# Kernel optimization log

Measured on AMD Instinct MI355X. Metric: run time of the kernel, lower is better.

## Reference

```python
import jax, jax.numpy as jnp
import numpy as np

N_NODES = 50000
N_EDGES = 800000
VOCAB = 10000
EMB = 128
HID = 128
OUT = 128
N_GRAPHS = 512


def setup_inputs() -> dict:
    key = jax.random.key(0)
    ks = jax.random.split(key, 12)
    edge_index = jax.random.randint(ks[0], (2, N_EDGES), 0, N_NODES, dtype=jnp.int64 if jax.config.jax_enable_x64 else jnp.int32)
    features = jax.random.randint(ks[1], (N_NODES, 1), 0, VOCAB, dtype=jnp.int32)
    batch = jnp.sort(jax.random.randint(ks[2], (N_NODES,), 0, N_GRAPHS, dtype=jnp.int32))
    s = 0.02
    emb = jax.random.normal(ks[3], (VOCAB, EMB), dtype=jnp.float32) * s
    W1 = jax.random.normal(ks[4], (EMB, HID), dtype=jnp.float32) * (1.0 / np.sqrt(EMB))
    b1 = jnp.zeros((HID,), dtype=jnp.float32)
    W2 = jax.random.normal(ks[5], (HID, HID), dtype=jnp.float32) * (1.0 / np.sqrt(HID))
    b2 = jnp.zeros((HID,), dtype=jnp.float32)
    W3 = jax.random.normal(ks[6], (HID, OUT), dtype=jnp.float32) * (1.0 / np.sqrt(HID))
    b3 = jnp.zeros((OUT,), dtype=jnp.float32)
    fcW = jax.random.normal(ks[7], (OUT, 1), dtype=jnp.float32) * (1.0 / np.sqrt(OUT))
    fcb = jnp.zeros((1,), dtype=jnp.float32)
    return dict(edge_index=edge_index, features=features, batch=batch,
                emb=emb, W1=W1, b1=b1, W2=W2, b2=b2, W3=W3, b3=b3,
                fcW=fcW, fcb=fcb)


def _gcn_conv(x, W, b, src, dst):
    # PyG GCNConv: add self-loops, symmetric deg^{-1/2} normalization,
    # linear transform first (no bias), then normalized scatter-add, then + bias.
    x = x @ W                                                    # [N, F_out]
    deg = jax.ops.segment_sum(jnp.ones((src.shape[0],), x.dtype), dst,
                              num_segments=N_NODES) + 1.0        # +1 self-loop
    dinv = jax.lax.rsqrt(deg)                                    # [N]
    norm = dinv[src] * dinv[dst]                                 # [E]
    msg = x[src] * norm[:, None]                                 # [E, F_out] gather
    agg = jax.ops.segment_sum(msg, dst, num_segments=N_NODES)    # scatter-add
    agg = agg + x * (dinv * dinv)[:, None]                       # self-loop term
    return agg + b


def reference(edge_index, features, batch, emb, W1, b1, W2, b2, W3, b3, fcW, fcb):
    src, dst = edge_index[0], edge_index[1]
    x = emb[features[:, 0]]                                      # [N, EMB]
    x = jax.nn.relu(_gcn_conv(x, W1, b1, src, dst))
    x = jax.nn.relu(_gcn_conv(x, W2, b2, src, dst))
    x = jax.nn.relu(_gcn_conv(x, W3, b3, src, dst))
    # global mean pool over graphs
    sums = jax.ops.segment_sum(x, batch, num_segments=N_GRAPHS)  # [G, OUT]
    cnts = jax.ops.segment_sum(jnp.ones((N_NODES,), x.dtype), batch,
                               num_segments=N_GRAPHS)
    pooled = sums / jnp.maximum(cnts, 1.0)[:, None]
    return (pooled @ fcW + fcb)[:, 0]                            # [G]
```

## Files before the change

kernel.cpp:

```cpp
#include <hip/hip_runtime.h>
#include <hip/hip_fp16.h>

#define N_NODES 50000
#define N_EDGES 800000
#define N_GRAPHS 512
#define VOCAB 10000
#define C 128
#define NBUCK 196
#define A_BLOCKS 200
#define EDGES_PER_A (N_EDGES / A_BLOCKS)
#define SE_CAP 8192

typedef __attribute__((ext_vector_type(8))) short short8v;
typedef __attribute__((ext_vector_type(4))) float f32x4;

__device__ __forceinline__ unsigned short f2bf(float f){
  unsigned u = __builtin_bit_cast(unsigned, f);
  unsigned r = u + 0x7FFFu + ((u >> 16) & 1u);
  return (unsigned short)(r >> 16);
}
__device__ __forceinline__ float bf2f(unsigned short h){
  unsigned u = ((unsigned)h) << 16;
  return __builtin_bit_cast(float, u);
}
__device__ __forceinline__ float h2f(short s){
  return __half2float(__builtin_bit_cast(__half, (unsigned short)s));
}

__global__ __launch_bounds__(256) void k_pre(const int* __restrict__ dst, int* __restrict__ blockHist,
                      const int* __restrict__ batch, int* __restrict__ gStart,
                      const float* __restrict__ W1, const float* __restrict__ W2,
                      const float* __restrict__ W3, short* __restrict__ Bp,
                      const float* __restrict__ emb, __half* __restrict__ embh){
  __shared__ int h[256];
  int b = blockIdx.x, t = threadIdx.x;
  if (b < A_BLOCKS){
    h[t] = 0; __syncthreads();
    int base = b * EDGES_PER_A;
    for (int i = t; i < EDGES_PER_A; i += 256)
      atomicAdd(&h[dst[base+i] >> 8], 1);
    __syncthreads();
    blockHist[t*A_BLOCKS + b] = h[t];
  } else if (b < A_BLOCKS+NBUCK){
    int i = (b-A_BLOCKS)*256 + t;
    if (i >= N_NODES) return;
    int bb = batch[i];
    int pb = (i==0) ? -1 : batch[i-1];
    for (int g=pb+1; g<=bb; g++) gStart[g] = i;
    if (i == N_NODES-1)
      for (int g=bb+1; g<=N_GRAPHS; g++) gStart[g] = N_NODES;
  } else if (b < A_BLOCKS+NBUCK+24){
    int idx = (b-A_BLOCKS-NBUCK)*256 + t;
    int layer = idx / 2048;
    int r = idx - layer*2048;
    const float* W = (layer==0) ? W1 : (layer==1) ? W2 : W3;
    short* Bh = Bp + (size_t)layer*32768;
    short* Bl = Bh + 16384;
    int lane = r & 63, tile = r >> 6;
    int kt = tile >> 3, ct = tile & 7;
    int q = lane >> 4, c = ct*16 + (lane & 15);
    #pragma unroll
    for (int i=0;i<8;i++){
      int k = kt*32 + q*8 + i;
      float w = W[k*C + c];
      unsigned short hh = f2bf(w);
      unsigned short ll = f2bf(w - bf2f(hh));
      Bh[(size_t)(tile*64 + lane)*8 + i] = (short)hh;
      Bl[(size_t)(tile*64 + lane)*8 + i] = (short)ll;
    }
  } else {
    int idx = (b-A_BLOCKS-NBUCK-24)*256 + t;
    const float2* s = (const float2*)emb;
    __half2* d2 = (__half2*)embh;
    for (int i = idx; i < VOCAB*C/2; i += 64*256)
      d2[i] = __float22half2_rn(s[i]);
  }
}

__global__ __launch_bounds__(64) void k_binScanA(const int* __restrict__ blockHist,
                        int* __restrict__ blockOfs, int* __restrict__ bucketTot){
  int b = blockIdx.x;
  int l = threadIdx.x;
  int carry = 0;
  for (int c = 0; c < 256; c += 64){
    int idx = c + l;
    int v = (idx < A_BLOCKS) ? blockHist[b*A_BLOCKS + idx] : 0;
    int x = v;
    #pragma unroll
    for (int off=1; off<64; off<<=1){
      int y = __shfl_up(x, off);
      if (l >= off) x += y;
    }
    if (idx < A_BLOCKS) blockOfs[b*A_BLOCKS + idx] = carry + x - v;
    carry += __shfl(x, 63);
  }
  if (l == 0) bucketTot[b] = carry;
}

__global__ __launch_bounds__(256) void k_binScatter(const int* __restrict__ src, const int* __restrict__ dst,
                           const int* __restrict__ bucketTot, const int* __restrict__ blockOfs,
                           unsigned* __restrict__ binned){
  __shared__ int s[256], ofs[256], cur[256];
  int t = threadIdx.x;
  int tv = bucketTot[t];
  s[t] = tv; __syncthreads();
  for (int off=1; off<256; off<<=1){
    int u = (t>=off) ? s[t-off] : 0;
    __syncthreads();
    s[t] += u;
    __syncthreads();
  }
  ofs[t] = (s[t] - tv) + blockOfs[t*A_BLOCKS + blockIdx.x];
  cur[t] = 0;
  __syncthreads();
  int base = blockIdx.x * EDGES_PER_A;
  for (int i = t; i < EDGES_PER_A; i += 256){
    int d = dst[base+i];
    int b = d >> 8;
    int p = atomicAdd(&cur[b], 1);
    binned[ofs[b] + p] = (unsigned)(src[base+i] & 0xFFFF) | ((unsigned)(d & 0xFF) << 16);
  }
}

__global__ __launch_bounds__(256) void k_binFinal(const unsigned* __restrict__ binned,
                         const int* __restrict__ bucketTot, const int* __restrict__ feat,
                         unsigned short* __restrict__ eSrc, unsigned short* __restrict__ eFeat,
                         int* __restrict__ rowStart, int* __restrict__ deg, float* __restrict__ dinv){
  __shared__ int h[256], pre[256], cur[256], excl[256];
  __shared__ unsigned short sE[SE_CAP];
  int b = blockIdx.x;
  int t = threadIdx.x;
  int tv = bucketTot[t];
  pre[t] = tv; __syncthreads();
  for (int off=1; off<256; off<<=1){
    int u = (t>=off) ? pre[t-off] : 0;
    __syncthreads();
    pre[t] += u;
    __syncthreads();
  }
  excl[t] = pre[t] - tv;
  __syncthreads();
  int base = excl[b], cnt = bucketTot[b];
  int nodeBase = b << 8;
  h[t] = 0; __syncthreads();
  for (int i = t; i < cnt; i += 256)
    atomicAdd(&h[binned[base+i] >> 16], 1);
  __syncthreads();
  pre[t] = h[t]; __syncthreads();
  for (int off=1; off<256; off<<=1){
    int u = (t>=off) ? pre[t-off] : 0;
    __syncthreads();
    pre[t] += u;
    __syncthreads();
  }
  int node = nodeBase + t;
  if (node < N_NODES){
    int d = h[t];
    deg[node] = d;
    rowStart[node] = base + pre[t] - d;
    dinv[node] = rsqrtf((float)d + 1.0f);
  }
  cur[t] = pre[t] - h[t];
  __syncthreads();
  for (int i = t; i < cnt; i += 256){
    unsigned v = binned[base+i];
    int dl = v >> 16;
    int p = atomicAdd(&cur[dl], 1);
    unsigned short s = (unsigned short)(v & 0xFFFF);
    if (p < SE_CAP) sE[p] = s;
    else eSrc[base + p] = s;
  }
  __syncthreads();
  int lim = cnt < SE_CAP ? cnt : SE_CAP;
  for (int i = t; i < lim; i += 256){
    unsigned short sv = sE[i];
    eSrc[base+i]  = sv;
    eFeat[base+i] = (unsigned short)feat[sv];
  }
  for (int i = SE_CAP + t; i < cnt; i += 256){
    eFeat[base+i] = (unsigned short)feat[eSrc[base+i]];
  }
}

__device__ __forceinline__ void store_split8(unsigned short* uh, unsigned short* ul,
                                             size_t node, int l16, const float* a){
  short8v hv, lv;
  #pragma unroll
  for (int i=0;i<8;i++){
    unsigned short hh = f2bf(a[i]);
    hv[i] = (short)hh;
    lv[i] = (short)f2bf(a[i] - bf2f(hh));
  }
  *(short8v*)&uh[node*C + l16*8] = hv;
  *(short8v*)&ul[node*C + l16*8] = lv;
}


__global__ __launch_bounds__(256) void k_agg1(const __half* __restrict__ embh,
                      const unsigned short* __restrict__ eSrc, const unsigned short* __restrict__ eFeat,
                      const int* __restrict__ rowStart, const int* __restrict__ deg,
                      const float* __restrict__ dinv, const int* __restrict__ feat,
                      unsigned short* __restrict__ uh, unsigned short* __restrict__ ul){
  int t = threadIdx.x;
  int wave = t>>6, lane = t&63;
  int sub = lane>>4, l16 = lane&15;
  int node = blockIdx.x*16 + wave*4 + sub;
  if (node >= N_NODES) return;
  int rs = rowStart[node], len = deg[node];
  float dn = dinv[node];
  const short8v* E = (const short8v*)embh;
  float a[8];
  {
    short8v v = E[(size_t)feat[node]*16 + l16];
    #pragma unroll
    for (int i=0;i<8;i++) a[i] = dn * h2f(v[i]);
  }
  int k = 0;
  for (; k+8<=len; k+=8){
    int f[8]; float dd[8];
    #pragma unroll
    for (int j=0;j<8;j++){
      int e = rs+k+j;
      f[j] = eFeat[e];
      dd[j] = dinv[eSrc[e]];
    }
    short8v v[8];
    #pragma unroll
    for (int j=0;j<8;j++) v[j] = E[(size_t)f[j]*16 + l16];
    #pragma unroll
    for (int j=0;j<8;j++)
      #pragma unroll
      for (int i=0;i<8;i++) a[i] = fmaf(dd[j], h2f(v[j][i]), a[i]);
  }
  for (; k<len; k++){
    float dd = dinv[eSrc[rs+k]];
    short8v v = E[(size_t)eFeat[rs+k]*16 + l16];
    #pragma unroll
    for (int i=0;i<8;i++) a[i] = fmaf(dd, h2f(v[i]), a[i]);
  }
  #pragma unroll
  for (int i=0;i<8;i++) a[i] *= dn;
  store_split8(uh, ul, (size_t)node, l16, a);
}


__global__ __launch_bounds__(256) void k_aggS(const __half* __restrict__ xs, const unsigned short* __restrict__ eSrc,
                      const int* __restrict__ rowStart, const int* __restrict__ deg,
                      const float* __restrict__ dinv,
                      unsigned short* __restrict__ uh, unsigned short* __restrict__ ul){
  int t = threadIdx.x;
  int wave = t>>6, lane = t&63;
  int sub = lane>>4, l16 = lane&15;
  int node = blockIdx.x*16 + wave*4 + sub;
  if (node >= N_NODES) return;
  int rs = rowStart[node], len = deg[node];
  const short8v* X = (const short8v*)xs;
  float a[8];
  {
    short8v v = X[(size_t)node*16 + l16];
    #pragma unroll
    for (int i=0;i<8;i++) a[i] = h2f(v[i]);
  }
  int k = 0;
  for (; k+8<=len; k+=8){
    int s[8];
    #pragma unroll
    for (int j=0;j<8;j++) s[j] = eSrc[rs+k+j];
    short8v v[8];
    #pragma unroll
    for (int j=0;j<8;j++) v[j] = X[(size_t)s[j]*16 + l16];
    #pragma unroll
    for (int j=0;j<8;j++)
      #pragma unroll
      for (int i=0;i<8;i++) a[i] += h2f(v[j][i]);
  }
  for (; k<len; k++){
    short8v v = X[(size_t)eSrc[rs+k]*16 + l16];
    #pragma unroll
    for (int i=0;i<8;i++) a[i] += h2f(v[i]);
  }
  float dn = dinv[node];
  #pragma unroll
  for (int i=0;i<8;i++) a[i] *= dn;
  store_split8(uh, ul, (size_t)node, l16, a);
}


__global__ __launch_bounds__(256) void k_gemmA(
            const unsigned short* __restrict__ uh, const unsigned short* __restrict__ ul,
            const short* __restrict__ Bh, const short* __restrict__ Bl,
            const float* __restrict__ bias, const float* __restrict__ dinv,
            __half* __restrict__ xs){
  int lane = threadIdx.x & 63;
  int pb = blockIdx.x*4 + (threadIdx.x >> 6);
  int R0 = pb*16;
  if (R0 >= N_NODES) return;
  int r15 = lane & 15, q = lane >> 4;
  int row = R0 + r15;
  const short8v* AH = (const short8v*)(uh + (size_t)row*C);
  const short8v* AL = (const short8v*)(ul + (size_t)row*C);
  const short8v* BH = (const short8v*)Bh;
  const short8v* BL = (const short8v*)Bl;
  f32x4 acc[8];
  #pragma unroll
  for (int ct=0;ct<8;ct++) acc[ct] = (f32x4){0.f,0.f,0.f,0.f};
  #pragma unroll
  for (int kt=0; kt<4; kt++){
    short8v ah = AH[kt*4 + q];
    short8v al = AL[kt*4 + q];
    #pragma unroll
    for (int ct=0; ct<8; ct++){
      short8v bh = BH[(kt*8+ct)*64 + lane];
      short8v bl = BL[(kt*8+ct)*64 + lane];
      acc[ct] = __builtin_amdgcn_mfma_f32_16x16x32_bf16(ah, bh, acc[ct], 0, 0, 0);
      acc[ct] = __builtin_amdgcn_mfma_f32_16x16x32_bf16(al, bh, acc[ct], 0, 0, 0);
      acc[ct] = __builtin_amdgcn_mfma_f32_16x16x32_bf16(ah, bl, acc[ct], 0, 0, 0);
    }
  }
  float bb[8];
  #pragma unroll
  for (int ct=0;ct<8;ct++) bb[ct] = bias[ct*16 + r15];
  #pragma unroll
  for (int j=0;j<4;j++){
    int rz = R0 + q*4 + j;
    float d = dinv[rz];
    #pragma unroll
    for (int ct=0; ct<8; ct++){
      float v = fmaxf(acc[ct][j] + bb[ct], 0.f);
      xs[(size_t)rz*C + ct*16 + r15] = __float2half(v * d);
    }
  }
}


__global__ __launch_bounds__(256) void k_gemm3(
            const unsigned short* __restrict__ uh, const unsigned short* __restrict__ ul,
            const short* __restrict__ Bh, const short* __restrict__ Bl,
            const float* __restrict__ bias, const float* __restrict__ fcW,
            float* __restrict__ dots){
  int lane = threadIdx.x & 63;
  int pb = blockIdx.x*4 + (threadIdx.x >> 6);
  int R0 = pb*16;
  if (R0 >= N_NODES) return;
  int r15 = lane & 15, q = lane >> 4;
  int row = R0 + r15;
  const short8v* AH = (const short8v*)(uh + (size_t)row*C);
  const short8v* AL = (const short8v*)(ul + (size_t)row*C);
  const short8v* BH = (const short8v*)Bh;
  const short8v* BL = (const short8v*)Bl;
  f32x4 acc[8];
  #pragma unroll
  for (int ct=0;ct<8;ct++) acc[ct] = (f32x4){0.f,0.f,0.f,0.f};
  #pragma unroll
  for (int kt=0; kt<4; kt++){
    short8v ah = AH[kt*4 + q];
    short8v al = AL[kt*4 + q];
    #pragma unroll
    for (int ct=0; ct<8; ct++){
      short8v bh = BH[(kt*8+ct)*64 + lane];
      short8v bl = BL[(kt*8+ct)*64 + lane];
      acc[ct] = __builtin_amdgcn_mfma_f32_16x16x32_bf16(ah, bh, acc[ct], 0, 0, 0);
      acc[ct] = __builtin_amdgcn_mfma_f32_16x16x32_bf16(al, bh, acc[ct], 0, 0, 0);
      acc[ct] = __builtin_amdgcn_mfma_f32_16x16x32_bf16(ah, bl, acc[ct], 0, 0, 0);
    }
  }
  float bb[8], fw[8];
  #pragma unroll
  for (int ct=0;ct<8;ct++){ bb[ct] = bias[ct*16 + r15]; fw[ct] = fcW[ct*16 + r15]; }
  #pragma unroll
  for (int j=0;j<4;j++){
    int rz = R0 + q*4 + j;
    float s = 0.f;
    #pragma unroll
    for (int ct=0; ct<8; ct++)
      s += fmaxf(acc[ct][j] + bb[ct], 0.f) * fw[ct];
    s += __shfl_xor(s, 1);
    s += __shfl_xor(s, 2);
    s += __shfl_xor(s, 4);
    s += __shfl_xor(s, 8);
    if (r15 == 0) dots[rz] = s;
  }
}


__global__ void k_pool_seg(const float* __restrict__ dots, const int* __restrict__ gStart,
                           const float* __restrict__ fcb, float* __restrict__ out){
  __shared__ float s[256];
  int g = blockIdx.x;
  int st = gStart[g], en = gStart[g+1];
  float acc = 0.f;
  for (int i = st + threadIdx.x; i < en; i += 256) acc += dots[i];
  s[threadIdx.x] = acc; __syncthreads();
  for (int off=128; off>0; off>>=1){
    if (threadIdx.x < off) s[threadIdx.x] += s[threadIdx.x+off];
    __syncthreads();
  }
  if (threadIdx.x==0) out[g] = s[0]/fmaxf((float)(en-st),1.0f) + fcb[0];
}


extern "C" void kernel_launch(void* const* d_in, const int* in_sizes, int n_in,
                              void* d_out, int out_size, void* d_ws, size_t ws_size,
                              hipStream_t stream){
  const int* edge  = (const int*)d_in[0];
  const int* srcI  = edge;
  const int* dstI  = edge + N_EDGES;
  const int* feat  = (const int*)d_in[1];
  const int* batch = (const int*)d_in[2];
  const float* emb = (const float*)d_in[3];
  const float* W1  = (const float*)d_in[4];
  const float* b1  = (const float*)d_in[5];
  const float* W2  = (const float*)d_in[6];
  const float* b2  = (const float*)d_in[7];
  const float* W3  = (const float*)d_in[8];
  const float* b3  = (const float*)d_in[9];
  const float* fcW = (const float*)d_in[10];
  const float* fcb = (const float*)d_in[11];
  float* out = (float*)d_out;

  __half* xs = (__half*)d_ws;
  unsigned short* uhp = (unsigned short*)(xs + (size_t)N_NODES*C);
  unsigned short* ulp = uhp + (size_t)N_NODES*C;
  __half* embh = (__half*)(ulp + (size_t)N_NODES*C);
  unsigned* binned = (unsigned*)(embh + (size_t)VOCAB*C);
  unsigned short* eSrc  = (unsigned short*)(binned + N_EDGES);
  unsigned short* eFeat = eSrc + N_EDGES;
  int* rowStart = (int*)(eFeat + N_EDGES);
  int* deg      = rowStart + N_NODES;
  float* dinv   = (float*)(deg + N_NODES);
  int* blockHist = (int*)(dinv + N_NODES);
  int* blockOfs  = blockHist + 256*A_BLOCKS;
  int* bucketTot = blockOfs + 256*A_BLOCKS;
  int* gStart    = bucketTot + 256;
  float* dots   = (float*)(gStart + 520);
  short* Bpack  = (short*)(dots + N_NODES);
  short* Bh1 = Bpack,           * Bl1 = Bpack + 16384;
  short* Bh2 = Bpack + 2*16384, * Bl2 = Bpack + 3*16384;
  short* Bh3 = Bpack + 4*16384, * Bl3 = Bpack + 5*16384;

  k_pre       <<<A_BLOCKS+NBUCK+24+64, 256, 0, stream>>>(dstI, blockHist, batch, gStart,
                                                         W1, W2, W3, Bpack, emb, embh);
  k_binScanA  <<<256, 64, 0, stream>>>(blockHist, blockOfs, bucketTot);
  k_binScatter<<<A_BLOCKS, 256, 0, stream>>>(srcI, dstI, bucketTot, blockOfs, binned);
  k_binFinal  <<<NBUCK, 256, 0, stream>>>(binned, bucketTot, feat, eSrc, eFeat,
                                          rowStart, deg, dinv);

  int aggBlocks  = (N_NODES+15)/16;
  int gemmBlocks = (N_NODES/16 + 3)/4;
  k_agg1 <<<aggBlocks, 256, 0, stream>>>(embh, eSrc, eFeat, rowStart, deg, dinv, feat, uhp, ulp);
  k_gemmA<<<gemmBlocks, 256, 0, stream>>>(uhp, ulp, Bh1, Bl1, b1, dinv, xs);
  k_aggS <<<aggBlocks, 256, 0, stream>>>(xs, eSrc, rowStart, deg, dinv, uhp, ulp);
  k_gemmA<<<gemmBlocks, 256, 0, stream>>>(uhp, ulp, Bh2, Bl2, b2, dinv, xs);
  k_aggS <<<aggBlocks, 256, 0, stream>>>(xs, eSrc, rowStart, deg, dinv, uhp, ulp);
  k_gemm3<<<gemmBlocks, 256, 0, stream>>>(uhp, ulp, Bh3, Bl3, b3, fcW, dots);

  k_pool_seg<<<N_GRAPHS, 256, 0, stream>>>(dots, gStart, fcb, out);
}
```

Measured before the change: 193.4 us.

## Fuse per-layer aggregation and GEMM into one kernel via LDS staging

Each GCN layer previously ran an aggregation kernel that wrote split bf16 hi/lo rows to global memory, followed by a separate MFMA GEMM kernel that read them back. The new templated kernel aggregates 16 nodes per block, stages the hi/lo split in swizzled shared memory, and has each of the four waves compute two of the eight output column tiles. This removes the global round trip of the intermediate and three kernel launches. The cost is that the GEMM work is spread more thinly per wave, and layer 2/3 now ping-pong between two feature buffers.

Measured after the change: 168.3 us. 1.15x faster.

```diff
diff --git a/kernel.cpp b/kernel.cpp
--- a/kernel.cpp
+++ b/kernel.cpp
@@ -182,203 +182,145 @@
   }
 }
 
-__device__ __forceinline__ void store_split8(unsigned short* uh, unsigned short* ul,
-                                             size_t node, int l16, const float* a){
-  short8v hv, lv;
-  #pragma unroll
-  for (int i=0;i<8;i++){
-    unsigned short hh = f2bf(a[i]);
-    hv[i] = (short)hh;
-    lv[i] = (short)f2bf(a[i] - bf2f(hh));
-  }
-  *(short8v*)&uh[node*C + l16*8] = hv;
-  *(short8v*)&ul[node*C + l16*8] = lv;
-}
-
-
-__global__ __launch_bounds__(256) void k_agg1(const __half* __restrict__ embh,
-                      const unsigned short* __restrict__ eSrc, const unsigned short* __restrict__ eFeat,
-                      const int* __restrict__ rowStart, const int* __restrict__ deg,
-                      const float* __restrict__ dinv, const int* __restrict__ feat,
-                      unsigned short* __restrict__ uh, unsigned short* __restrict__ ul){
+
+template<int LAYER>
+__global__ __launch_bounds__(256) void k_layer(
+      const __half* __restrict__ gsrc,
+      const unsigned short* __restrict__ eSrc, const unsigned short* __restrict__ eFeat,
+      const int* __restrict__ rowStart, const int* __restrict__ deg,
+      const float* __restrict__ dinv, const int* __restrict__ feat,
+      const short* __restrict__ Bh, const short* __restrict__ Bl,
+      const float* __restrict__ bias, const float* __restrict__ fcW,
+      __half* __restrict__ xsOut, float* __restrict__ dots){
+  __shared__ unsigned short uhl[16*C];
+  __shared__ unsigned short ull[16*C];
+  __shared__ float dotb[16][4];
   int t = threadIdx.x;
   int wave = t>>6, lane = t&63;
   int sub = lane>>4, l16 = lane&15;
-  int node = blockIdx.x*16 + wave*4 + sub;
-  if (node >= N_NODES) return;
-  int rs = rowStart[node], len = deg[node];
-  float dn = dinv[node];
-  const short8v* E = (const short8v*)embh;
+  int node0 = blockIdx.x*16;
+  int r = wave*4 + sub;
+  int node = node0 + r;
+
   float a[8];
   {
-    short8v v = E[(size_t)feat[node]*16 + l16];
-    #pragma unroll
-    for (int i=0;i<8;i++) a[i] = dn * h2f(v[i]);
-  }
-  int k = 0;
-  for (; k+8<=len; k+=8){
-    int f[8]; float dd[8];
-    #pragma unroll
-    for (int j=0;j<8;j++){
-      int e = rs+k+j;
-      f[j] = eFeat[e];
-      dd[j] = dinv[eSrc[e]];
-    }
-    short8v v[8];
-    #pragma unroll
-    for (int j=0;j<8;j++) v[j] = E[(size_t)f[j]*16 + l16];
-    #pragma unroll
-    for (int j=0;j<8;j++)
+    int rs = rowStart[node], len = deg[node];
+    float dn = dinv[node];
+    const short8v* X = (const short8v*)gsrc;
+    if (LAYER == 1){
+      short8v v = X[(size_t)feat[node]*16 + l16];
       #pragma unroll
-      for (int i=0;i<8;i++) a[i] = fmaf(dd[j], h2f(v[j][i]), a[i]);
-  }
-  for (; k<len; k++){
-    float dd = dinv[eSrc[rs+k]];
-    short8v v = E[(size_t)eFeat[rs+k]*16 + l16];
-    #pragma unroll
-    for (int i=0;i<8;i++) a[i] = fmaf(dd, h2f(v[i]), a[i]);
-  }
-  #pragma unroll
-  for (int i=0;i<8;i++) a[i] *= dn;
-  store_split8(uh, ul, (size_t)node, l16, a);
-}
-
-
-__global__ __launch_bounds__(256) void k_aggS(const __half* __restrict__ xs, const unsigned short* __restrict__ eSrc,
-                      const int* __restrict__ rowStart, const int* __restrict__ deg,
-                      const float* __restrict__ dinv,
-                      unsigned short* __restrict__ uh, unsigned short* __restrict__ ul){
-  int t = threadIdx.x;
-  int wave = t>>6, lane = t&63;
-  int sub = lane>>4, l16 = lane&15;
-  int node = blockIdx.x*16 + wave*4 + sub;
-  if (node >= N_NODES) return;
-  int rs = rowStart[node], len = deg[node];
-  const short8v* X = (const short8v*)xs;
-  float a[8];
+      for (int i=0;i<8;i++) a[i] = dn * h2f(v[i]);
+      int k = 0;
+      for (; k+8<=len; k+=8){
+        int f[8]; float dd[8];
+        #pragma unroll
+        for (int j=0;j<8;j++){
+          int e = rs+k+j;
+          f[j] = eFeat[e];
+          dd[j] = dinv[eSrc[e]];
+        }
+        short8v v8[8];
+        #pragma unroll
+        for (int j=0;j<8;j++) v8[j] = X[(size_t)f[j]*16 + l16];
+        #pragma unroll
+        for (int j=0;j<8;j++)
+          #pragma unroll
+          for (int i=0;i<8;i++) a[i] = fmaf(dd[j], h2f(v8[j][i]), a[i]);
+      }
+      for (; k<len; k++){
+        float dd = dinv[eSrc[rs+k]];
+        short8v v1 = X[(size_t)eFeat[rs+k]*16 + l16];
+        #pragma unroll
+        for (int i=0;i<8;i++) a[i] = fmaf(dd, h2f(v1[i]), a[i]);
+      }
+    } else {
+      short8v v = X[(size_t)node*16 + l16];
+      #pragma unroll
+      for (int i=0;i<8;i++) a[i] = h2f(v[i]);
+      int k = 0;
+      for (; k+8<=len; k+=8){
+        int s[8];
+        #pragma unroll
+        for (int j=0;j<8;j++) s[j] = eSrc[rs+k+j];
+        short8v v8[8];
+        #pragma unroll
+        for (int j=0;j<8;j++) v8[j] = X[(size_t)s[j]*16 + l16];
+        #pragma unroll
+        for (int j=0;j<8;j++)
+          #pragma unroll
+          for (int i=0;i<8;i++) a[i] += h2f(v8[j][i]);
+      }
+      for (; k<len; k++){
+        short8v v1 = X[(size_t)eSrc[rs+k]*16 + l16];
+        #pragma unroll
+        for (int i=0;i<8;i++) a[i] += h2f(v1[i]);
+      }
+    }
+    #pragma unroll
+    for (int i=0;i<8;i++) a[i] *= dn;
+  }
   {
-    short8v v = X[(size_t)node*16 + l16];
-    #pragma unroll
-    for (int i=0;i<8;i++) a[i] = h2f(v[i]);
-  }
-  int k = 0;
-  for (; k+8<=len; k+=8){
-    int s[8];
-    #pragma unroll
-    for (int j=0;j<8;j++) s[j] = eSrc[rs+k+j];
-    short8v v[8];
-    #pragma unroll
-    for (int j=0;j<8;j++) v[j] = X[(size_t)s[j]*16 + l16];
-    #pragma unroll
-    for (int j=0;j<8;j++)
-      #pragma unroll
-      for (int i=0;i<8;i++) a[i] += h2f(v[j][i]);
-  }
-  for (; k<len; k++){
-    short8v v = X[(size_t)eSrc[rs+k]*16 + l16];
-    #pragma unroll
-    for (int i=0;i<8;i++) a[i] += h2f(v[i]);
-  }
-  float dn = dinv[node];
-  #pragma unroll
-  for (int i=0;i<8;i++) a[i] *= dn;
-  store_split8(uh, ul, (size_t)node, l16, a);
-}
-
-
-__global__ __launch_bounds__(256) void k_gemmA(
-            const unsigned short* __restrict__ uh, const unsigned short* __restrict__ ul,
-            const short* __restrict__ Bh, const short* __restrict__ Bl,
-            const float* __restrict__ bias, const float* __restrict__ dinv,
-            __half* __restrict__ xs){
-  int lane = threadIdx.x & 63;
-  int pb = blockIdx.x*4 + (threadIdx.x >> 6);
-  int R0 = pb*16;
-  if (R0 >= N_NODES) return;
+    short8v hv, lv;
+    #pragma unroll
+    for (int i=0;i<8;i++){
+      unsigned short hh = f2bf(a[i]);
+      hv[i] = (short)hh;
+      lv[i] = (short)f2bf(a[i] - bf2f(hh));
+    }
+    unsigned boff = (unsigned)(r*256 + l16*16) ^ ((unsigned)(r&7)<<4);
+    *(short8v*)((char*)uhl + boff) = hv;
+    *(short8v*)((char*)ull + boff) = lv;
+  }
+  __syncthreads();
+
   int r15 = lane & 15, q = lane >> 4;
-  int row = R0 + r15;
-  const short8v* AH = (const short8v*)(uh + (size_t)row*C);
-  const short8v* AL = (const short8v*)(ul + (size_t)row*C);
   const short8v* BH = (const short8v*)Bh;
   const short8v* BL = (const short8v*)Bl;
-  f32x4 acc[8];
-  #pragma unroll
-  for (int ct=0;ct<8;ct++) acc[ct] = (f32x4){0.f,0.f,0.f,0.f};
+  f32x4 acc[2];
+  acc[0] = (f32x4){0.f,0.f,0.f,0.f};
+  acc[1] = (f32x4){0.f,0.f,0.f,0.f};
   #pragma unroll
   for (int kt=0; kt<4; kt++){
-    short8v ah = AH[kt*4 + q];
-    short8v al = AL[kt*4 + q];
-    #pragma unroll
-    for (int ct=0; ct<8; ct++){
+    unsigned boff = (unsigned)(r15*256 + (kt*4+q)*16) ^ ((unsigned)(r15&7)<<4);
+    short8v ah = *(const short8v*)((const char*)uhl + boff);
+    short8v al = *(const short8v*)((const char*)ull + boff);
+    #pragma unroll
+    for (int c=0;c<2;c++){
+      int ct = wave*2 + c;
       short8v bh = BH[(kt*8+ct)*64 + lane];
       short8v bl = BL[(kt*8+ct)*64 + lane];
-      acc[ct] = __builtin_amdgcn_mfma_f32_16x16x32_bf16(ah, bh, acc[ct], 0, 0, 0);
-      acc[ct] = __builtin_amdgcn_mfma_f32_16x16x32_bf16(al, bh, acc[ct], 0, 0, 0);
-      acc[ct] = __builtin_amdgcn_mfma_f32_16x16x32_bf16(ah, bl, acc[ct], 0, 0, 0);
-    }
-  }
-  float bb[8];
-  #pragma unroll
-  for (int ct=0;ct<8;ct++) bb[ct] = bias[ct*16 + r15];
-  #pragma unroll
-  for (int j=0;j<4;j++){
-    int rz = R0 + q*4 + j;
-    float d = dinv[rz];
-    #pragma unroll
-    for (int ct=0; ct<8; ct++){
-      float v = fmaxf(acc[ct][j] + bb[ct], 0.f);
-      xs[(size_t)rz*C + ct*16 + r15] = __float2half(v * d);
-    }
-  }
-}
-
-
-__global__ __launch_bounds__(256) void k_gemm3(
-            const unsigned short* __restrict__ uh, const unsigned short* __restrict__ ul,
-            const short* __restrict__ Bh, const short* __restrict__ Bl,
-            const float* __restrict__ bias, const float* __restrict__ fcW,
-            float* __restrict__ dots){
-  int lane = threadIdx.x & 63;
-  int pb = blockIdx.x*4 + (threadIdx.x >> 6);
-  int R0 = pb*16;
-  if (R0 >= N_NODES) return;
-  int r15 = lane & 15, q = lane >> 4;
-  int row = R0 + r15;
-  const short8v* AH = (const short8v*)(uh + (size_t)row*C);
-  const short8v* AL = (const short8v*)(ul + (size_t)row*C);
-  const short8v* BH = (const short8v*)Bh;
-  const short8v* BL = (const short8v*)Bl;
-  f32x4 acc[8];
-  #pragma unroll
-  for (int ct=0;ct<8;ct++) acc[ct] = (f32x4){0.f,0.f,0.f,0.f};
-  #pragma unroll
-  for (int kt=0; kt<4; kt++){
-    short8v ah = AH[kt*4 + q];
-    short8v al = AL[kt*4 + q];
-    #pragma unroll
-    for (int ct=0; ct<8; ct++){
-      short8v bh = BH[(kt*8+ct)*64 + lane];
-      short8v bl = BL[(kt*8+ct)*64 + lane];
-      acc[ct] = __builtin_amdgcn_mfma_f32_16x16x32_bf16(ah, bh, acc[ct], 0, 0, 0);
-      acc[ct] = __builtin_amdgcn_mfma_f32_16x16x32_bf16(al, bh, acc[ct], 0, 0, 0);
-      acc[ct] = __builtin_amdgcn_mfma_f32_16x16x32_bf16(ah, bl, acc[ct], 0, 0, 0);
-    }
-  }
-  float bb[8], fw[8];
-  #pragma unroll
-  for (int ct=0;ct<8;ct++){ bb[ct] = bias[ct*16 + r15]; fw[ct] = fcW[ct*16 + r15]; }
-  #pragma unroll
-  for (int j=0;j<4;j++){
-    int rz = R0 + q*4 + j;
-    float s = 0.f;
-    #pragma unroll
-    for (int ct=0; ct<8; ct++)
-      s += fmaxf(acc[ct][j] + bb[ct], 0.f) * fw[ct];
-    s += __shfl_xor(s, 1);
-    s += __shfl_xor(s, 2);
-    s += __shfl_xor(s, 4);
-    s += __shfl_xor(s, 8);
-    if (r15 == 0) dots[rz] = s;
+      acc[c] = __builtin_amdgcn_mfma_f32_16x16x32_bf16(ah, bh, acc[c], 0, 0, 0);
+      acc[c] = __builtin_amdgcn_mfma_f32_16x16x32_bf16(al, bh, acc[c], 0, 0, 0);
+      acc[c] = __builtin_amdgcn_mfma_f32_16x16x32_bf16(ah, bl, acc[c], 0, 0, 0);
+    }
+  }
+  float bb[2] = { bias[(wave*2)*16 + r15], bias[(wave*2+1)*16 + r15] };
+  if (LAYER == 3){
+    float fw[2] = { fcW[(wave*2)*16 + r15], fcW[(wave*2+1)*16 + r15] };
+    #pragma unroll
+    for (int j=0;j<4;j++){
+      float s = fmaxf(acc[0][j] + bb[0], 0.f)*fw[0]
+              + fmaxf(acc[1][j] + bb[1], 0.f)*fw[1];
+      s += __shfl_xor(s, 1);
+      s += __shfl_xor(s, 2);
+      s += __shfl_xor(s, 4);
+      s += __shfl_xor(s, 8);
+      if (r15 == 0) dotb[q*4 + j][wave] = s;
+    }
+    __syncthreads();
+    if (t < 16) dots[node0 + t] = dotb[t][0] + dotb[t][1] + dotb[t][2] + dotb[t][3];
+  } else {
+    #pragma unroll
+    for (int j=0;j<4;j++){
+      int rz = node0 + q*4 + j;
+      float d = dinv[rz];
+      #pragma unroll
+      for (int c=0;c<2;c++){
+        float v = fmaxf(acc[c][j] + bb[c], 0.f);
+        xsOut[(size_t)rz*C + (wave*2+c)*16 + r15] = __float2half(v * d);
+      }
+    }
   }
 }
 
@@ -418,10 +360,9 @@
   const float* fcb = (const float*)d_in[11];
   float* out = (float*)d_out;
 
-  __half* xs = (__half*)d_ws;
-  unsigned short* uhp = (unsigned short*)(xs + (size_t)N_NODES*C);
-  unsigned short* ulp = uhp + (size_t)N_NODES*C;
-  __half* embh = (__half*)(ulp + (size_t)N_NODES*C);
+  __half* xsA = (__half*)d_ws;
+  __half* xsB = xsA + (size_t)N_NODES*C;
+  __half* embh = xsB + (size_t)N_NODES*C;
   unsigned* binned = (unsigned*)(embh + (size_t)VOCAB*C);
   unsigned short* eSrc  = (unsigned short*)(binned + N_EDGES);
   unsigned short* eFeat = eSrc + N_EDGES;
@@ -445,14 +386,13 @@
   k_binFinal  <<<NBUCK, 256, 0, stream>>>(binned, bucketTot, feat, eSrc, eFeat,
                                           rowStart, deg, dinv);
 
-  int aggBlocks  = (N_NODES+15)/16;
-  int gemmBlocks = (N_NODES/16 + 3)/4;
-  k_agg1 <<<aggBlocks, 256, 0, stream>>>(embh, eSrc, eFeat, rowStart, deg, dinv, feat, uhp, ulp);
-  k_gemmA<<<gemmBlocks, 256, 0, stream>>>(uhp, ulp, Bh1, Bl1, b1, dinv, xs);
-  k_aggS <<<aggBlocks, 256, 0, stream>>>(xs, eSrc, rowStart, deg, dinv, uhp, ulp);
-  k_gemmA<<<gemmBlocks, 256, 0, stream>>>(uhp, ulp, Bh2, Bl2, b2, dinv, xs);
-  k_aggS <<<aggBlocks, 256, 0, stream>>>(xs, eSrc, rowStart, deg, dinv, uhp, ulp);
-  k_gemm3<<<gemmBlocks, 256, 0, stream>>>(uhp, ulp, Bh3, Bl3, b3, fcW, dots);
+  int LBLOCKS = N_NODES/16;
+  k_layer<1><<<LBLOCKS, 256, 0, stream>>>(embh, eSrc, eFeat, rowStart, deg, dinv, feat,
+                                          Bh1, Bl1, b1, nullptr, xsB, nullptr);
+  k_layer<2><<<LBLOCKS, 256, 0, stream>>>(xsB, eSrc, nullptr, rowStart, deg, dinv, nullptr,
+                                          Bh2, Bl2, b2, nullptr, xsA, nullptr);
+  k_layer<3><<<LBLOCKS, 256, 0, stream>>>(xsA, eSrc, nullptr, rowStart, deg, dinv, nullptr,
+                                          Bh3, Bl3, b3, fcW, nullptr, dots);
 
   k_pool_seg<<<N_GRAPHS, 256, 0, stream>>>(dots, gStart, fcb, out);
 }
```

## Slice node features into 16-channel planes for cache-local gather aggregation

Applied to the files above, without the earlier changes.

Node features become eight channel-slice planes, each 50000x16 fp16 (about 1.6 MB per slice), and every aggregation block works on a single slice. The aim is to keep the randomly gathered neighbour rows resident in L2 instead of fetching full 256-byte rows from HBM. The layer-1 embedding gather pre-scaled by dinv is moved into k_binFinal, which drops the eFeat array and the dedicated k_agg1 kernel so all three layers share one aggregation kernel. The cost is that edge indices are re-read once per slice, eight times in all, plus a masked tail loop and an extra feature buffer in the workspace.

Measured after the change: 217.4 us. 12.4% more time.

```diff
diff --git a/kernel.cpp b/kernel.cpp
--- a/kernel.cpp
+++ b/kernel.cpp
@@ -10,6 +10,8 @@
 #define A_BLOCKS 200
 #define EDGES_PER_A (N_EDGES / A_BLOCKS)
 #define SE_CAP 8192
+#define NSLICE 8
+#define SLICE_H ((size_t)N_NODES*16)
 
 typedef __attribute__((ext_vector_type(8))) short short8v;
 typedef __attribute__((ext_vector_type(4))) float f32x4;
@@ -124,9 +126,11 @@
 
 __global__ __launch_bounds__(256) void k_binFinal(const unsigned* __restrict__ binned,
                          const int* __restrict__ bucketTot, const int* __restrict__ feat,
-                         unsigned short* __restrict__ eSrc, unsigned short* __restrict__ eFeat,
+                         const __half* __restrict__ embh,
+                         unsigned short* __restrict__ eSrc, __half* __restrict__ xs0,
                          int* __restrict__ rowStart, int* __restrict__ deg, float* __restrict__ dinv){
   __shared__ int h[256], pre[256], cur[256], excl[256];
+  __shared__ float dinvS[256];
   __shared__ unsigned short sE[SE_CAP];
   int b = blockIdx.x;
   int t = threadIdx.x;
@@ -154,12 +158,15 @@
     __syncthreads();
   }
   int node = nodeBase + t;
+  float dn = 0.f;
   if (node < N_NODES){
     int d = h[t];
     deg[node] = d;
     rowStart[node] = base + pre[t] - d;
-    dinv[node] = rsqrtf((float)d + 1.0f);
-  }
+    dn = rsqrtf((float)d + 1.0f);
+    dinv[node] = dn;
+  }
+  dinvS[t] = dn;
   cur[t] = pre[t] - h[t];
   __syncthreads();
   for (int i = t; i < cnt; i += 256){
@@ -172,95 +179,42 @@
   }
   __syncthreads();
   int lim = cnt < SE_CAP ? cnt : SE_CAP;
-  for (int i = t; i < lim; i += 256){
-    unsigned short sv = sE[i];
-    eSrc[base+i]  = sv;
-    eFeat[base+i] = (unsigned short)feat[sv];
-  }
-  for (int i = SE_CAP + t; i < cnt; i += 256){
-    eFeat[base+i] = (unsigned short)feat[eSrc[base+i]];
-  }
-}
-
-__device__ __forceinline__ void store_split8(unsigned short* uh, unsigned short* ul,
-                                             size_t node, int l16, const float* a){
-  short8v hv, lv;
-  #pragma unroll
-  for (int i=0;i<8;i++){
-    unsigned short hh = f2bf(a[i]);
-    hv[i] = (short)hh;
-    lv[i] = (short)f2bf(a[i] - bf2f(hh));
-  }
-  *(short8v*)&uh[node*C + l16*8] = hv;
-  *(short8v*)&ul[node*C + l16*8] = lv;
-}
-
-
-__global__ __launch_bounds__(256) void k_agg1(const __half* __restrict__ embh,
-                      const unsigned short* __restrict__ eSrc, const unsigned short* __restrict__ eFeat,
-                      const int* __restrict__ rowStart, const int* __restrict__ deg,
-                      const float* __restrict__ dinv, const int* __restrict__ feat,
-                      unsigned short* __restrict__ uh, unsigned short* __restrict__ ul){
-  int t = threadIdx.x;
-  int wave = t>>6, lane = t&63;
-  int sub = lane>>4, l16 = lane&15;
-  int node = blockIdx.x*16 + wave*4 + sub;
-  if (node >= N_NODES) return;
-  int rs = rowStart[node], len = deg[node];
-  float dn = dinv[node];
-  const short8v* E = (const short8v*)embh;
-  float a[8];
-  {
-    short8v v = E[(size_t)feat[node]*16 + l16];
-    #pragma unroll
-    for (int i=0;i<8;i++) a[i] = dn * h2f(v[i]);
-  }
-  int k = 0;
-  for (; k+8<=len; k+=8){
-    int f[8]; float dd[8];
-    #pragma unroll
-    for (int j=0;j<8;j++){
-      int e = rs+k+j;
-      f[j] = eFeat[e];
-      dd[j] = dinv[eSrc[e]];
-    }
-    short8v v[8];
-    #pragma unroll
-    for (int j=0;j<8;j++) v[j] = E[(size_t)f[j]*16 + l16];
-    #pragma unroll
-    for (int j=0;j<8;j++)
+  for (int i = t; i < lim; i += 256) eSrc[base+i] = sE[i];
+  int l16 = t & 15;
+  for (int n = t >> 4; n < 256; n += 16){
+    int nd = nodeBase + n;
+    if (nd < N_NODES){
+      short8v v = ((const short8v*)embh)[(size_t)feat[nd]*16 + l16];
+      float d = dinvS[n];
+      short8v o;
       #pragma unroll
-      for (int i=0;i<8;i++) a[i] = fmaf(dd[j], h2f(v[j][i]), a[i]);
-  }
-  for (; k<len; k++){
-    float dd = dinv[eSrc[rs+k]];
-    short8v v = E[(size_t)eFeat[rs+k]*16 + l16];
-    #pragma unroll
-    for (int i=0;i<8;i++) a[i] = fmaf(dd, h2f(v[i]), a[i]);
-  }
-  #pragma unroll
-  for (int i=0;i<8;i++) a[i] *= dn;
-  store_split8(uh, ul, (size_t)node, l16, a);
-}
-
-
-__global__ __launch_bounds__(256) void k_aggS(const __half* __restrict__ xs, const unsigned short* __restrict__ eSrc,
+      for (int i=0;i<8;i++)
+        o[i] = (short)__builtin_bit_cast(unsigned short, __float2half(d * h2f(v[i])));
+      ((short8v*)xs0)[(size_t)(l16>>1)*((size_t)N_NODES*2) + (size_t)nd*2 + (l16&1)] = o;
+    }
+  }
+}
+
+
+__global__ __launch_bounds__(256) void k_aggSl(const __half* __restrict__ gsrc_sl,
+                      const unsigned short* __restrict__ eSrc,
                       const int* __restrict__ rowStart, const int* __restrict__ deg,
                       const float* __restrict__ dinv,
                       unsigned short* __restrict__ uh, unsigned short* __restrict__ ul){
   int t = threadIdx.x;
-  int wave = t>>6, lane = t&63;
-  int sub = lane>>4, l16 = lane&15;
-  int node = blockIdx.x*16 + wave*4 + sub;
+  int slice = blockIdx.x & 7;
+  int tile  = blockIdx.x >> 3;
+  int half  = t & 1;
+  int node  = tile*128 + (t >> 1);
   if (node >= N_NODES) return;
-  int rs = rowStart[node], len = deg[node];
-  const short8v* X = (const short8v*)xs;
+  const short8v* X = (const short8v*)gsrc_sl + (size_t)slice*((size_t)N_NODES*2);
   float a[8];
   {
-    short8v v = X[(size_t)node*16 + l16];
-    #pragma unroll
-    for (int i=0;i<8;i++) a[i] = h2f(v[i]);
-  }
+    short8v sv = X[(size_t)node*2 + half];
+    #pragma unroll
+    for (int i=0;i<8;i++) a[i] = h2f(sv[i]);
+  }
+  int rs = rowStart[node], len = deg[node];
   int k = 0;
   for (; k+8<=len; k+=8){
     int s[8];
@@ -268,21 +222,39 @@
     for (int j=0;j<8;j++) s[j] = eSrc[rs+k+j];
     short8v v[8];
     #pragma unroll
-    for (int j=0;j<8;j++) v[j] = X[(size_t)s[j]*16 + l16];
+    for (int j=0;j<8;j++) v[j] = X[(size_t)s[j]*2 + half];
     #pragma unroll
     for (int j=0;j<8;j++)
       #pragma unroll
       for (int i=0;i<8;i++) a[i] += h2f(v[j][i]);
   }
-  for (; k<len; k++){
-    short8v v = X[(size_t)eSrc[rs+k]*16 + l16];
-    #pragma unroll
-    for (int i=0;i<8;i++) a[i] += h2f(v[i]);
+  int rem = len - k;
+  if (rem > 0){
+    int sR[7]; short8v vR[7];
+    #pragma unroll
+    for (int j=0;j<7;j++) sR[j] = (j < rem) ? (int)eSrc[rs+k+j] : node;
+    #pragma unroll
+    for (int j=0;j<7;j++) vR[j] = X[(size_t)sR[j]*2 + half];
+    #pragma unroll
+    for (int j=0;j<7;j++){
+      if (j < rem){
+        #pragma unroll
+        for (int i=0;i<8;i++) a[i] += h2f(vR[j][i]);
+      }
+    }
   }
   float dn = dinv[node];
-  #pragma unroll
-  for (int i=0;i<8;i++) a[i] *= dn;
-  store_split8(uh, ul, (size_t)node, l16, a);
+  short8v hv, lv;
+  #pragma unroll
+  for (int i=0;i<8;i++){
+    float f = a[i] * dn;
+    unsigned short hh = f2bf(f);
+    hv[i] = (short)hh;
+    lv[i] = (short)f2bf(f - bf2f(hh));
+  }
+  size_t uidx = (size_t)node*16 + slice*2 + half;
+  ((short8v*)uh)[uidx] = hv;
+  ((short8v*)ul)[uidx] = lv;
 }
 
 
@@ -290,7 +262,7 @@
             const unsigned short* __restrict__ uh, const unsigned short* __restrict__ ul,
             const short* __restrict__ Bh, const short* __restrict__ Bl,
             const float* __restrict__ bias, const float* __restrict__ dinv,
-            __half* __restrict__ xs){
+            __half* __restrict__ xsOut){
   int lane = threadIdx.x & 63;
   int pb = blockIdx.x*4 + (threadIdx.x >> 6);
   int R0 = pb*16;
@@ -327,7 +299,7 @@
     #pragma unroll
     for (int ct=0; ct<8; ct++){
       float v = fmaxf(acc[ct][j] + bb[ct], 0.f);
-      xs[(size_t)rz*C + ct*16 + r15] = __float2half(v * d);
+      xsOut[(size_t)ct*SLICE_H + (size_t)rz*16 + r15] = __float2half(v * d);
     }
   }
 }
@@ -418,14 +390,15 @@
   const float* fcb = (const float*)d_in[11];
   float* out = (float*)d_out;
 
-  __half* xs = (__half*)d_ws;
-  unsigned short* uhp = (unsigned short*)(xs + (size_t)N_NODES*C);
+  __half* xsA = (__half*)d_ws;
+  __half* xsB = xsA + (size_t)N_NODES*C;
+  __half* xs0 = xsB + (size_t)N_NODES*C;
+  unsigned short* uhp = (unsigned short*)(xs0 + (size_t)N_NODES*C);
   unsigned short* ulp = uhp + (size_t)N_NODES*C;
   __half* embh = (__half*)(ulp + (size_t)N_NODES*C);
   unsigned* binned = (unsigned*)(embh + (size_t)VOCAB*C);
   unsigned short* eSrc  = (unsigned short*)(binned + N_EDGES);
-  unsigned short* eFeat = eSrc + N_EDGES;
-  int* rowStart = (int*)(eFeat + N_EDGES);
+  int* rowStart = (int*)(eSrc + N_EDGES);
   int* deg      = rowStart + N_NODES;
   float* dinv   = (float*)(deg + N_NODES);
   int* blockHist = (int*)(dinv + N_NODES);
@@ -442,16 +415,16 @@
                                                          W1, W2, W3, Bpack, emb, embh);
   k_binScanA  <<<256, 64, 0, stream>>>(blockHist, blockOfs, bucketTot);
   k_binScatter<<<A_BLOCKS, 256, 0, stream>>>(srcI, dstI, bucketTot, blockOfs, binned);
-  k_binFinal  <<<NBUCK, 256, 0, stream>>>(binned, bucketTot, feat, eSrc, eFeat,
+  k_binFinal  <<<NBUCK, 256, 0, stream>>>(binned, bucketTot, feat, embh, eSrc, xs0,
                                           rowStart, deg, dinv);
 
-  int aggBlocks  = (N_NODES+15)/16;
+  int aggBlocks  = NSLICE * ((N_NODES + 127)/128);
   int gemmBlocks = (N_NODES/16 + 3)/4;
-  k_agg1 <<<aggBlocks, 256, 0, stream>>>(embh, eSrc, eFeat, rowStart, deg, dinv, feat, uhp, ulp);
-  k_gemmA<<<gemmBlocks, 256, 0, stream>>>(uhp, ulp, Bh1, Bl1, b1, dinv, xs);
-  k_aggS <<<aggBlocks, 256, 0, stream>>>(xs, eSrc, rowStart, deg, dinv, uhp, ulp);
-  k_gemmA<<<gemmBlocks, 256, 0, stream>>>(uhp, ulp, Bh2, Bl2, b2, dinv, xs);
-  k_aggS <<<aggBlocks, 256, 0, stream>>>(xs, eSrc, rowStart, deg, dinv, uhp, ulp);
+  k_aggSl<<<aggBlocks, 256, 0, stream>>>(xs0, eSrc, rowStart, deg, dinv, uhp, ulp);
+  k_gemmA<<<gemmBlocks, 256, 0, stream>>>(uhp, ulp, Bh1, Bl1, b1, dinv, xsB);
+  k_aggSl<<<aggBlocks, 256, 0, stream>>>(xsB, eSrc, rowStart, deg, dinv, uhp, ulp);
+  k_gemmA<<<gemmBlocks, 256, 0, stream>>>(uhp, ulp, Bh2, Bl2, b2, dinv, xsA);
+  k_aggSl<<<aggBlocks, 256, 0, stream>>>(xsA, eSrc, rowStart, deg, dinv, uhp, ulp);
   k_gemm3<<<gemmBlocks, 256, 0, stream>>>(uhp, ulp, Bh3, Bl3, b3, fcW, dots);
 
   k_pool_seg<<<N_GRAPHS, 256, 0, stream>>>(dots, gStart, fcb, out);
```
